# Performance work log

Hardware: AMD Instinct MI355X
Metric: run time of the kernel (lower is better)

## Reference

```python
import jax, jax.numpy as jnp
import numpy as np

B, T, C, H = 2, 2048, 1024, 16
N = C // H
MISS_ROWS = 128


def _rwkv7_scan(q, w_log, k, v, a, b):
    # all [B,T,H,N] float32 (bf16-rounded). RWKV7 delta-rule recurrence:
    #   S_t = S_{t-1} * diag(exp(w_t)) + (S_{t-1} a_t) b_t^T + v_t k_t^T
    #   o_t = S_t q_t   (state S has shape [B,H,Nv,Nk]; decay along k-dim)
    Bq, Tq, Hq, Nq = q.shape

    def step(S, inp):
        q_t, w_t, k_t, v_t, a_t, b_t = inp
        ew = jnp.exp(w_t)  # decay in (0,1) since w_log = -exp(...) < 0
        sa = jnp.einsum('bhvi,bhi->bhv', S, a_t)
        S = S * ew[:, :, None, :] + sa[..., None] * b_t[:, :, None, :] + v_t[..., None] * k_t[:, :, None, :]
        o = jnp.einsum('bhvj,bhj->bhv', S, q_t)
        return S, o

    xs = tuple(jnp.moveaxis(u, 1, 0) for u in (q, w_log, k, v, a, b))
    S0 = jnp.zeros((Bq, Hq, Nq, Nq), jnp.float32)
    _, o = jax.lax.scan(step, S0, xs)
    return jnp.moveaxis(o, 0, 1)  # [B,T,H,N]


def setup_inputs() -> dict:
    key = jax.random.key(0)
    ks = jax.random.split(key, 16)
    f32 = jnp.float32
    return {
        'residual': jax.random.normal(ks[0], (B, T, C), f32),
        'x': jax.random.normal(ks[1], (B, T, C), f32),
        'x0': jax.random.normal(ks[2], (B, T, C), f32),
        'dx0': jax.random.normal(ks[3], (B, T, C), f32),
        'Wq': jax.random.normal(ks[4], (C, C), f32) * 0.02,
        'Wk': jax.random.normal(ks[5], (C, C), f32) * 0.02,
        'Wv': jax.random.normal(ks[6], (C, C), f32) * 0.02,
        'Wproj': jax.random.normal(ks[7], (C, C), f32) * 0.02,
        'x_q': jax.random.uniform(ks[8], (1, 1, C), f32),
        'x_k': jax.random.uniform(ks[9], (1, 1, C), f32),
        'x_v': jax.random.uniform(ks[10], (1, 1, C), f32),
        'v0': 0.7 + 0.1 * jax.random.normal(ks[11], (1, 1, C), f32),
        'w0': -3.0 + 0.5 * jax.random.normal(ks[12], (1, 1, C), f32),
        'a0': 0.1 * jax.random.normal(ks[13], (1, 1, C), f32),
        'miss': jax.random.normal(ks[14], (MISS_ROWS, 4 * C), f32) * 0.02,
        'r_k': 0.1 * jax.random.normal(ks[15], (H, N), f32),
    }


def reference(residual, x, x0, dx0, Wq, Wk, Wv, Wproj, x_q, x_k, x_v, v0, w0, a0, miss, r_k):
    Bx, Tx, Cx = x.shape
    Hh, Nn = r_k.shape
    # token shift: dx_prev = x_{t-1} - x_t (zero-padded at t=0)
    dx_prev = jnp.concatenate([jnp.zeros_like(x[:, :1]), x[:, :-1]], axis=1) - x
    q = (x + dx_prev * x_q) @ Wq.T
    k = (x + dx_prev * x_k) @ Wk.T
    v = (x + dx_prev * x_v) @ Wv.T
    deltas = x[:, :, :miss.shape[0]] @ miss  # [B,T,4C]
    w_delta, v_delta, a_delta, g = jnp.split(deltas, 4, axis=-1)
    log_neglog_w = -jax.nn.softplus(-(w0 + w_delta)) - 0.5
    log_w = -jnp.exp(log_neglog_w)  # log decay, always < 0
    v_first = (x0 + dx0 * x_v) @ Wv.T
    v = v + (v_first - v) * jax.nn.sigmoid(v0 + v_delta)
    g = 1.0 + g
    a = jax.nn.sigmoid(a0 + a_delta)
    kh = k.reshape(Bx, Tx, Hh, Nn)
    kk = kh / jnp.maximum(jnp.linalg.norm(kh, axis=-1, keepdims=True), 1e-12)
    kk = kk.reshape(Bx, Tx, Cx)
    k = k * a
    z = -kk
    b = kk * a
    bf = lambda u: u.astype(jnp.bfloat16).astype(jnp.float32).reshape(Bx, Tx, Hh, Nn)
    qh, wh, kh2, vh, zh, bh = (bf(u) for u in (q, log_w, k, v, z, b))
    y = _rwkv7_scan(qh, wh, kh2, vh, zh, bh) * (float(Nn) ** -0.5)  # [B,T,H,N]
    xnorm = jnp.linalg.norm(x.reshape(Bx, Tx, Hh, Nn), axis=-1, keepdims=True)
    vnorm = jnp.linalg.norm(vh, axis=-1, keepdims=True)
    u = (1.0 - xnorm / (vnorm + 1e-12)) * jax.nn.sigmoid(r_k)
    y = (y + vh * u).reshape(Bx, Tx, Cx)
    y = y * g
    return residual + y @ Wproj.T
```

## Files before the change

### kernel.cpp

```cpp
#include <hip/hip_runtime.h>
#include <stdint.h>
#include <stddef.h>

#define B_ 2
#define T_ 2048
#define C_ 1024
#define H_ 16
#define N_ 64
#define M_ (B_*T_)
#define L_ 128
#define NC_ (T_/L_)

typedef unsigned short ushort_t;
typedef __attribute__((ext_vector_type(8))) __bf16 bf16x8;
typedef __attribute__((ext_vector_type(4))) float  f32x4;

__device__ __forceinline__ ushort_t f2bf(float x){
  uint32_t u = __float_as_uint(x);
  u += 0x7fffu + ((u >> 16) & 1u);
  return (ushort_t)(u >> 16);
}
__device__ __forceinline__ float bf2f(uint32_t hu){
  return __uint_as_float(hu << 16);
}
__device__ __forceinline__ void ldbf16x16(const ushort_t* p, float* o){
  uint4 u0 = *(const uint4*)p;
  uint4 u1 = *(const uint4*)(p+8);
  o[0]=bf2f(u0.x&0xffffu); o[1]=bf2f(u0.x>>16);
  o[2]=bf2f(u0.y&0xffffu); o[3]=bf2f(u0.y>>16);
  o[4]=bf2f(u0.z&0xffffu); o[5]=bf2f(u0.z>>16);
  o[6]=bf2f(u0.w&0xffffu); o[7]=bf2f(u0.w>>16);
  o[8]=bf2f(u1.x&0xffffu); o[9]=bf2f(u1.x>>16);
  o[10]=bf2f(u1.y&0xffffu); o[11]=bf2f(u1.y>>16);
  o[12]=bf2f(u1.z&0xffffu); o[13]=bf2f(u1.z>>16);
  o[14]=bf2f(u1.w&0xffffu); o[15]=bf2f(u1.w>>16);
}
__device__ __forceinline__ float quad_sum(float v){
  float a = __int_as_float(__builtin_amdgcn_mov_dpp(__float_as_int(v), 0xB1, 0xF, 0xF, true));
  v += a;
  float b = __int_as_float(__builtin_amdgcn_mov_dpp(__float_as_int(v), 0x4E, 0xF, 0xF, true));
  return v + b;
}

__device__ __forceinline__ ushort4 mixq4(float4 a, float4 p, float4 c){
  ushort4 o;
  o.x = f2bf(fmaf(p.x - a.x, c.x, a.x));
  o.y = f2bf(fmaf(p.y - a.y, c.y, a.y));
  o.z = f2bf(fmaf(p.z - a.z, c.z, a.z));
  o.w = f2bf(fmaf(p.w - a.w, c.w, a.w));
  return o;
}
__global__ __launch_bounds__(256) void prep_all(
    const float* __restrict__ x, const float* __restrict__ x0,
    const float* __restrict__ dx0,
    const float* __restrict__ xq, const float* __restrict__ xk,
    const float* __restrict__ xv,
    const float* __restrict__ Wq, const float* __restrict__ Wk,
    const float* __restrict__ Wv, const float* __restrict__ Wp,
    const float* __restrict__ miss,
    ushort_t* __restrict__ Aq, ushort_t* __restrict__ Ak,
    ushort_t* __restrict__ Av, ushort_t* __restrict__ Axf,
    ushort_t* __restrict__ Xb,
    ushort_t* __restrict__ Wb, ushort_t* __restrict__ Wpb,
    ushort_t* __restrict__ missT)
{
  __shared__ ushort_t tile[128][66];
  const int blk = blockIdx.x;
  const int tid = threadIdx.x;
  if (blk < 4096){
    const int idx = blk*256 + tid;
    const int col4 = idx & 255;
    const int i = idx >> 8;
    const int t = i & (T_-1);
    float4 a = ((const float4*)x)[idx];
    float4 p = {0.f,0.f,0.f,0.f};
    if (t > 0) p = ((const float4*)x)[idx - 256];
    float4 cq = ((const float4*)xq)[col4];
    float4 ck = ((const float4*)xk)[col4];
    float4 cv = ((const float4*)xv)[col4];
    ((ushort4*)Aq)[idx] = mixq4(a, p, cq);
    ((ushort4*)Ak)[idx] = mixq4(a, p, ck);
    ((ushort4*)Av)[idx] = mixq4(a, p, cv);
    float4 z = ((const float4*)x0)[idx];
    float4 d = ((const float4*)dx0)[idx];
    ushort4 of;
    of.x = f2bf(fmaf(d.x, cv.x, z.x));
    of.y = f2bf(fmaf(d.y, cv.y, z.y));
    of.z = f2bf(fmaf(d.z, cv.z, z.z));
    of.w = f2bf(fmaf(d.w, cv.w, z.w));
    ((ushort4*)Axf)[idx] = of;
    ushort4 ob = {f2bf(a.x), f2bf(a.y), f2bf(a.z), f2bf(a.w)};
    ((ushort4*)Xb)[idx] = ob;
  } else if (blk < 4096 + 5*1024){
    const int y = (blk - 4096) >> 10;
    const float* src = (y==0)?Wq:(y==1)?Wk:(y<4)?Wv:Wp;
    ushort_t* dst = (y<4) ? Wb + (size_t)y*C_*C_ : Wpb;
    const int idx = ((blk - 4096) & 1023)*256 + tid;
    float4 v = ((const float4*)src)[idx];
    ushort4 o = {f2bf(v.x), f2bf(v.y), f2bf(v.z), f2bf(v.w)};
    ((ushort4*)dst)[idx] = o;
  } else {
    const int j0 = (blk - 4096 - 5*1024)*64;
#pragma unroll
    for (int rep=0; rep<8; rep++){
      int k = rep*16 + (tid>>4);
      int jj = (tid&15)*4;
      float4 v = *(const float4*)&miss[(size_t)k*4096 + j0 + jj];
      tile[k][jj+0]=f2bf(v.x); tile[k][jj+1]=f2bf(v.y);
      tile[k][jj+2]=f2bf(v.z); tile[k][jj+3]=f2bf(v.w);
    }
    __syncthreads();
#pragma unroll
    for (int rep=0; rep<8; rep++){
      int j = tid>>2;
      int kk = (tid&3)*32 + rep*4;
      ushort4 o = {tile[kk+0][j], tile[kk+1][j], tile[kk+2][j], tile[kk+3][j]};
      *(ushort4*)&missT[(size_t)(j0+j)*128 + kk] = o;
    }
  }
}

__global__ __launch_bounds__(256, 2) void mfma_gemm(
    const ushort_t* __restrict__ Ab, int lda, int64_t Asz,
    const ushort_t* __restrict__ Bbp, int ldb, int64_t Bsz,
    void* __restrict__ Cb, int ldc, int64_t Csz, int c_bf16,
    const float* __restrict__ resid, int K)
{
  const ushort_t* A  = Ab  + (size_t)blockIdx.z * Asz;
  const ushort_t* Bm = Bbp + (size_t)blockIdx.z * Bsz;
  const int i0 = blockIdx.y * 128;
  const int j0 = blockIdx.x * 128;
  const int tid = threadIdx.x;
  const int lane = tid & 63;
  const int w = tid >> 6;
  const int wm = w & 1, wn = w >> 1;

  __shared__ ushort_t As[128*32];
  __shared__ ushort_t Bs[128*32];

  f32x4 acc[4][4];
#pragma unroll
  for (int i=0;i<4;i++)
#pragma unroll
    for (int j=0;j<4;j++) acc[i][j] = (f32x4){0.f,0.f,0.f,0.f};

  const int lr = lane >> 2;
  const int ls = lane & 3;
  const ushort_t* ga = A  + (size_t)(i0 + w*32 + lr)*lda + ls*8;
  const ushort_t* gb = Bm + (size_t)(j0 + w*32 + lr)*ldb + ls*8;
  const int lm = lane & 15, lq = lane >> 4;

  for (int k0 = 0; k0 < K; k0 += 32){
    __syncthreads();
#pragma unroll
    for (int p=0;p<2;p++){
      __builtin_amdgcn_global_load_lds(
        (const __attribute__((address_space(1))) void*)(ga + (size_t)p*16*lda + k0),
        (__attribute__((address_space(3))) void*)&As[(w*32 + p*16)*32], 16, 0, 0);
      __builtin_amdgcn_global_load_lds(
        (const __attribute__((address_space(1))) void*)(gb + (size_t)p*16*ldb + k0),
        (__attribute__((address_space(3))) void*)&Bs[(w*32 + p*16)*32], 16, 0, 0);
    }
    __syncthreads();
    bf16x8 af[4], bfr[4];
#pragma unroll
    for (int i=0;i<4;i++)
      af[i] = *(const bf16x8*)&As[(wm*64 + i*16 + lm)*32 + lq*8];
#pragma unroll
    for (int j=0;j<4;j++)
      bfr[j] = *(const bf16x8*)&Bs[(wn*64 + j*16 + lm)*32 + lq*8];
#pragma unroll
    for (int i=0;i<4;i++)
#pragma unroll
      for (int j=0;j<4;j++)
        acc[i][j] = __builtin_amdgcn_mfma_f32_16x16x32_bf16(af[i], bfr[j], acc[i][j], 0, 0, 0);
  }

  if (!c_bf16){
    float* C = (float*)Cb + (size_t)blockIdx.z * Csz;
#pragma unroll
    for (int i=0;i<4;i++)
#pragma unroll
      for (int j=0;j<4;j++)
#pragma unroll
        for (int r=0;r<4;r++){
          const int row = i0 + wm*64 + i*16 + lq*4 + r;
          const int col = j0 + wn*64 + j*16 + lm;
          float v = acc[i][j][r];
          if (resid) v += resid[(size_t)row*ldc + col];
          C[(size_t)row*ldc + col] = v;
        }
  } else {
    ushort_t* C = (ushort_t*)Cb + (size_t)blockIdx.z * Csz;
#pragma unroll
    for (int i=0;i<4;i++)
#pragma unroll
      for (int j=0;j<4;j++)
#pragma unroll
        for (int r=0;r<4;r++){
          const int row = i0 + wm*64 + i*16 + lq*4 + r;
          const int col = j0 + wn*64 + j*16 + lm;
          C[(size_t)row*ldc + col] = f2bf(acc[i][j][r]);
        }
  }
}

__global__ __launch_bounds__(256) void fuse_kernel(
    const float* __restrict__ qm, const float* __restrict__ km,
    const float* __restrict__ vm, const float* __restrict__ vfm,
    const ushort_t* __restrict__ del, const float* __restrict__ x,
    const float* __restrict__ w0, const float* __restrict__ v0,
    const float* __restrict__ a0,
    uint32_t* __restrict__ packed, float* __restrict__ gout,
    float* __restrict__ ratio)
{
  const int lane = threadIdx.x & 63;
  const int ht = blockIdx.x*4 + (threadIdx.x >> 6);
  const int i = ht >> 4;
  const int h = ht & 15;
  const int c = h*64 + lane;
  const size_t ic = (size_t)i*C_ + c;
  float qv = qm[ic], kv = km[ic], vv = vm[ic], vfv = vfm[ic], xv = x[ic];
  const size_t d0 = (size_t)i*4*C_ + c;
  float wd = bf2f(del[d0]), vd = bf2f(del[d0+C_]);
  float ad = bf2f(del[d0+2*C_]), gd = bf2f(del[d0+3*C_]);

  float z1 = -(w0[c]+wd);
  float sp = fmaxf(z1, 0.f) + log1pf(expf(-fabsf(z1)));
  float logw = -expf(-sp - 0.5f);
  float sv = 1.f/(1.f+expf(-(v0[c]+vd)));
  vv = vv + (vfv - vv)*sv;
  float gv = 1.f + gd;
  float av = 1.f/(1.f+expf(-(a0[c]+ad)));

  ushort_t vr_u = f2bf(vv);
  float vrf = bf2f(vr_u);

  float ksq = kv*kv, xsq = xv*xv, vsq = vrf*vrf;
#pragma unroll
  for (int off=32; off>0; off>>=1){
    ksq += __shfl_xor(ksq, off, 64);
    xsq += __shfl_xor(xsq, off, 64);
    vsq += __shfl_xor(vsq, off, 64);
  }
  float kn = sqrtf(ksq);
  float kkn = kv / fmaxf(kn, 1e-12f);
  float k2 = kv*av;
  float zv = -kkn;
  float bv = kkn*av;

  uint32_t p0 = (uint32_t)f2bf(logw) | ((uint32_t)f2bf(zv) << 16);
  uint32_t p1 = (uint32_t)f2bf(bv)   | ((uint32_t)f2bf(k2) << 16);
  uint32_t p2 = (uint32_t)f2bf(qv)   | ((uint32_t)vr_u << 16);
  uint32_t* pb = packed + ((size_t)ht*64 + lane)*3;
  pb[0]=p0; pb[1]=p1; pb[2]=p2;
  gout[ic] = gv;
  if (lane == 0)
    ratio[ht] = 1.f - sqrtf(xsq)/(sqrtf(vsq)+1e-12f);
}


__global__ __launch_bounds__(512, 4) void chunk_mdp_kernel(
    const uint32_t* __restrict__ packed,
    float* __restrict__ phi, float* __restrict__ cc, float* __restrict__ md)
{
  const int tid  = threadIdx.x;
  const int role = tid >> 8;
  const int row  = (tid >> 2) & 63;
  const int qr   = tid & 3;

  __shared__ float ewS[8][N_], zS[8][N_], bS[8][N_], kS[8][N_], qS[8][N_], vS[8][N_];

  const int g  = blockIdx.x;
  const int cx = g & (NC_-1), bh = g >> 4;
  const int b = bh >> 4, h = bh & 15;
  const size_t pbase = ((size_t)(b*T_ + cx*L_)*H_ + h)*64;

  const int ls = tid >> 6;
  const int ld = tid & 63;

  uint32_t pu0, pu1, pu2;
  {
    size_t ap = (pbase + (size_t)ls*(H_*64) + ld)*3;
    pu0 = packed[ap]; pu1 = packed[ap+1]; pu2 = packed[ap+2];
  }

  float R[16];
  if (role == 0){
#pragma unroll
    for (int i=0;i<16;i++) R[i] = (qr*16+i == row) ? 1.f : 0.f;
  } else {
#pragma unroll
    for (int i=0;i<16;i++) R[i] = 0.f;
  }

  for (int tg = 0; tg < L_; tg += 8){
    __syncthreads();
    ewS[ls][ld] = __expf(bf2f(pu0 & 0xffffu));
    zS[ls][ld]  = bf2f(pu0 >> 16);
    bS[ls][ld]  = bf2f(pu1 & 0xffffu);
    kS[ls][ld]  = bf2f(pu1 >> 16);
    qS[ls][ld]  = bf2f(pu2 & 0xffffu);
    vS[ls][ld]  = bf2f(pu2 >> 16);
    if (tg + 8 < L_){
      size_t ap = (pbase + (size_t)(tg+8+ls)*(H_*64) + ld)*3;
      pu0 = packed[ap]; pu1 = packed[ap+1]; pu2 = packed[ap+2];
    }
    __syncthreads();
#pragma unroll 1
    for (int ss=0; ss<8; ss++){
      const float* zr = &zS[ss][qr*16];
      float s_ = 0.f;
#pragma unroll
      for (int i4=0;i4<4;i4++){
        float4 z4 = *(const float4*)&zr[i4*4];
        s_ = fmaf(R[i4*4+0], z4.x, s_);
        s_ = fmaf(R[i4*4+1], z4.y, s_);
        s_ = fmaf(R[i4*4+2], z4.z, s_);
        s_ = fmaf(R[i4*4+3], z4.w, s_);
      }
      s_ = quad_sum(s_);
      const float* er = &ewS[ss][qr*16];
      const float* br = &bS[ss][qr*16];
      const float* qrp = &qS[ss][qr*16];
      float o = 0.f;
      if (role == 0){
#pragma unroll
        for (int i4=0;i4<4;i4++){
          float4 e4 = *(const float4*)&er[i4*4];
          float4 b4 = *(const float4*)&br[i4*4];
          float4 q4 = *(const float4*)&qrp[i4*4];
          float t;
          t = fmaf(R[i4*4+0], e4.x, s_*b4.x); R[i4*4+0]=t; o = fmaf(t, q4.x, o);
          t = fmaf(R[i4*4+1], e4.y, s_*b4.y); R[i4*4+1]=t; o = fmaf(t, q4.y, o);
          t = fmaf(R[i4*4+2], e4.z, s_*b4.z); R[i4*4+2]=t; o = fmaf(t, q4.z, o);
          t = fmaf(R[i4*4+3], e4.w, s_*b4.w); R[i4*4+3]=t; o = fmaf(t, q4.w, o);
        }
      } else {
        const float* kr = &kS[ss][qr*16];
        const float vr = vS[ss][row];
#pragma unroll
        for (int i4=0;i4<4;i4++){
          float4 e4 = *(const float4*)&er[i4*4];
          float4 b4 = *(const float4*)&br[i4*4];
          float4 q4 = *(const float4*)&qrp[i4*4];
          float4 k4 = *(const float4*)&kr[i4*4];
          float t;
          t = fmaf(R[i4*4+0], e4.x, fmaf(s_, b4.x, vr*k4.x)); R[i4*4+0]=t; o = fmaf(t, q4.x, o);
          t = fmaf(R[i4*4+1], e4.y, fmaf(s_, b4.y, vr*k4.y)); R[i4*4+1]=t; o = fmaf(t, q4.y, o);
          t = fmaf(R[i4*4+2], e4.z, fmaf(s_, b4.z, vr*k4.z)); R[i4*4+2]=t; o = fmaf(t, q4.z, o);
          t = fmaf(R[i4*4+3], e4.w, fmaf(s_, b4.w, vr*k4.w)); R[i4*4+3]=t; o = fmaf(t, q4.w, o);
        }
      }
      o = quad_sum(o);
      if (qr == 0)
        md[((size_t)g*L_ + tg+ss)*128 + role*64 + row] = o;
    }
  }
  float* dst = (role == 0) ? phi : cc;
  const size_t base = (size_t)g*4096 + (size_t)row*64 + qr*16;
#pragma unroll
  for (int i4=0;i4<4;i4++)
    *(float4*)&dst[base + i4*4] = (float4){R[i4*4+0],R[i4*4+1],R[i4*4+2],R[i4*4+3]};
}

__global__ __launch_bounds__(256) void chunk_state_kernel(
    const float* __restrict__ phi, const float* __restrict__ cc,
    float* __restrict__ sstart)
{
  const int bh = blockIdx.x;
  const int tid = threadIdx.x;
  const int rb = tid >> 4;
  const int cq = tid & 15;
  __shared__ float Sld[64][65];
  __shared__ float Fld[64][68];
  float acc[4][4];
#pragma unroll
  for (int m=0;m<4;m++)
#pragma unroll
    for (int i=0;i<4;i++) acc[m][i] = 0.f;
#pragma unroll
  for (int m=0;m<4;m++){
    float4 z4 = {0.f,0.f,0.f,0.f};
    *(float4*)&Sld[rb+16*m][cq*4] = z4;
  }
  const float* pc = phi + (size_t)bh*NC_*4096;
  const float* cb = cc  + (size_t)bh*NC_*4096;
  float4 pf[4], pcc[4];
#pragma unroll
  for (int p=0;p<4;p++) pf[p] = *(const float4*)&pc[(size_t)p*1024 + tid*4];
#pragma unroll
  for (int m=0;m<4;m++) pcc[m] = *(const float4*)&cb[(size_t)(rb+16*m)*64 + cq*4];

  for (int c=0;c<NC_;c++){
    __syncthreads();
#pragma unroll
    for (int p=0;p<4;p++){
      int f = p*1024 + tid*4;
      *(float4*)&Fld[f>>6][f&63] = pf[p];
    }
    float na[4][4];
#pragma unroll
    for (int m=0;m<4;m++){
      na[m][0]=pcc[m].x; na[m][1]=pcc[m].y; na[m][2]=pcc[m].z; na[m][3]=pcc[m].w;
    }
#pragma unroll
    for (int m=0;m<4;m++){
      float4 so = {acc[m][0],acc[m][1],acc[m][2],acc[m][3]};
      *(float4*)&sstart[(size_t)(bh*NC_+c)*4096 + (size_t)(rb+16*m)*64 + cq*4] = so;
    }
    if (c+1 < NC_){
#pragma unroll
      for (int p=0;p<4;p++) pf[p] = *(const float4*)&pc[(size_t)(c+1)*4096 + p*1024 + tid*4];
#pragma unroll
      for (int m=0;m<4;m++) pcc[m] = *(const float4*)&cb[(size_t)(c+1)*4096 + (size_t)(rb+16*m)*64 + cq*4];
    }
    __syncthreads();
#pragma unroll 1
    for (int k0=0;k0<64;k0+=4){
      float4 sr[4];
#pragma unroll
      for (int m=0;m<4;m++) sr[m] = *(const float4*)&Sld[rb+16*m][k0];
      const float4 f0 = *(const float4*)&Fld[k0+0][cq*4];
      const float4 f1 = *(const float4*)&Fld[k0+1][cq*4];
      const float4 f2 = *(const float4*)&Fld[k0+2][cq*4];
      const float4 f3 = *(const float4*)&Fld[k0+3][cq*4];
#pragma unroll
      for (int m=0;m<4;m++){
        na[m][0] = fmaf(sr[m].x, f0.x, na[m][0]); na[m][0] = fmaf(sr[m].y, f1.x, na[m][0]);
        na[m][0] = fmaf(sr[m].z, f2.x, na[m][0]); na[m][0] = fmaf(sr[m].w, f3.x, na[m][0]);
        na[m][1] = fmaf(sr[m].x, f0.y, na[m][1]); na[m][1] = fmaf(sr[m].y, f1.y, na[m][1]);
        na[m][1] = fmaf(sr[m].z, f2.y, na[m][1]); na[m][1] = fmaf(sr[m].w, f3.y, na[m][1]);
        na[m][2] = fmaf(sr[m].x, f0.z, na[m][2]); na[m][2] = fmaf(sr[m].y, f1.z, na[m][2]);
        na[m][2] = fmaf(sr[m].z, f2.z, na[m][2]); na[m][2] = fmaf(sr[m].w, f3.z, na[m][2]);
        na[m][3] = fmaf(sr[m].x, f0.w, na[m][3]); na[m][3] = fmaf(sr[m].y, f1.w, na[m][3]);
        na[m][3] = fmaf(sr[m].z, f2.w, na[m][3]); na[m][3] = fmaf(sr[m].w, f3.w, na[m][3]);
      }
    }
    __syncthreads();
#pragma unroll
    for (int m=0;m<4;m++){
      float4 so = {na[m][0],na[m][1],na[m][2],na[m][3]};
      *(float4*)&Sld[rb+16*m][cq*4] = so;
#pragma unroll
      for (int i=0;i<4;i++) acc[m][i] = na[m][i];
    }
  }
}

__global__ __launch_bounds__(256) void chunk_emit_kernel(
    const uint32_t* __restrict__ packed, const float* __restrict__ ratio,
    const float* __restrict__ g, const float* __restrict__ rk,
    const float* __restrict__ sstart, const float* __restrict__ md,
    ushort_t* __restrict__ y)
{
  const int blk = blockIdx.x;
  const int c  = blk & (NC_-1);
  const int bh = blk >> 4;
  const int b = bh >> 4, h = bh & 15;
  const int tid = threadIdx.x;
  const int v = tid & 63;
  const int tg = tid >> 6;

  float4 sr[16];
  const float4* sp = (const float4*)(sstart + (size_t)blk*4096 + (size_t)v*64);
#pragma unroll
  for (int f=0;f<16;f++) sr[f] = sp[f];
  const float sigrk = 1.f/(1.f+__expf(-rk[h*64+v]));

#pragma unroll 1
  for (int ss=0; ss<32; ss++){
    const int t = tg*32 + ss;
    const int token = b*T_ + c*L_ + t;
    const float* mrow = md + ((size_t)blk*L_ + t)*128;
    float o0=0.f,o1=0.f,o2=0.f,o3=0.f;
#pragma unroll
    for (int f=0;f<16;f+=4){
      float4 m0 = ((const float4*)mrow)[f+0];
      float4 m1 = ((const float4*)mrow)[f+1];
      float4 m2 = ((const float4*)mrow)[f+2];
      float4 m3 = ((const float4*)mrow)[f+3];
      o0 = fmaf(sr[f+0].x,m0.x, fmaf(sr[f+0].y,m0.y, fmaf(sr[f+0].z,m0.z, fmaf(sr[f+0].w,m0.w, o0))));
      o1 = fmaf(sr[f+1].x,m1.x, fmaf(sr[f+1].y,m1.y, fmaf(sr[f+1].z,m1.z, fmaf(sr[f+1].w,m1.w, o1))));
      o2 = fmaf(sr[f+2].x,m2.x, fmaf(sr[f+2].y,m2.y, fmaf(sr[f+2].z,m2.z, fmaf(sr[f+2].w,m2.w, o2))));
      o3 = fmaf(sr[f+3].x,m3.x, fmaf(sr[f+3].y,m3.y, fmaf(sr[f+3].z,m3.z, fmaf(sr[f+3].w,m3.w, o3))));
    }
    float o = ((o0+o1)+(o2+o3)) + mrow[64 + v];
    const float vt = bf2f(packed[(((size_t)token*H_ + h)*64 + v)*3 + 2] >> 16);
    const float uv = ratio[(size_t)token*H_ + h];
    const float gv = g[(size_t)token*C_ + h*64 + v];
    y[(size_t)token*C_ + h*64 + v] = f2bf((o*0.125f + vt*uv*sigrk)*gv);
  }
}

extern "C" void kernel_launch(void* const* d_in, const int* in_sizes, int n_in,
                              void* d_out, int out_size, void* d_ws, size_t ws_size,
                              hipStream_t stream)
{
  const float* residual = (const float*)d_in[0];
  const float* x    = (const float*)d_in[1];
  const float* x0   = (const float*)d_in[2];
  const float* dx0  = (const float*)d_in[3];
  const float* Wq   = (const float*)d_in[4];
  const float* Wk   = (const float*)d_in[5];
  const float* Wv   = (const float*)d_in[6];
  const float* Wpr  = (const float*)d_in[7];
  const float* x_q  = (const float*)d_in[8];
  const float* x_k  = (const float*)d_in[9];
  const float* x_v  = (const float*)d_in[10];
  const float* v0   = (const float*)d_in[11];
  const float* w0   = (const float*)d_in[12];
  const float* a0   = (const float*)d_in[13];
  const float* miss = (const float*)d_in[14];
  const float* rk   = (const float*)d_in[15];
  float* out = (float*)d_out;

  char* ws = (char*)d_ws;
  const size_t MB = (size_t)1 << 20;
  float*    q_m    = (float*)(ws + 0*MB);
  float*    k_m    = (float*)(ws + 16*MB);
  float*    v_m    = (float*)(ws + 32*MB);
  float*    vf_m   = (float*)(ws + 48*MB);
  ushort_t* delb   = (ushort_t*)(ws + 64*MB);
  ushort_t* Ab     = (ushort_t*)(ws + 96*MB);
  ushort_t* Xb     = (ushort_t*)(ws + 128*MB);
  ushort_t* Wb     = (ushort_t*)(ws + 136*MB);
  uint32_t* packed = (uint32_t*)(ws + 96*MB);
  float*    g_m    = (float*)(ws + 144*MB);
  ushort_t* Wpb    = (ushort_t*)(ws + 160*MB);
  ushort_t* missT  = (ushort_t*)(ws + 162*MB);
  float*    ratio  = (float*)(ws + 163*MB);
  float*    phi    = (float*)(ws + 0*MB);
  float*    cc     = (float*)(ws + 16*MB);
  float*    sstart = (float*)(ws + 32*MB);
  ushort_t* yb     = (ushort_t*)(ws + 48*MB);
  float*    mdbuf  = (float*)(ws + 64*MB);

  ushort_t* Aq  = Ab + 0*(size_t)M_*C_;
  ushort_t* Ak  = Ab + 1*(size_t)M_*C_;
  ushort_t* Av  = Ab + 2*(size_t)M_*C_;
  ushort_t* Axf = Ab + 3*(size_t)M_*C_;

  dim3 blk(256);
  prep_all<<<4096 + 5*1024 + 64, blk, 0, stream>>>(
      x, x0, dx0, x_q, x_k, x_v, Wq, Wk, Wv, Wpr, miss,
      Aq, Ak, Av, Axf, Xb, Wb, Wpb, missT);
  mfma_gemm<<<dim3(C_/128, M_/128, 4), blk, 0, stream>>>(
      Ab, C_, (int64_t)M_*C_, Wb, C_, (int64_t)C_*C_,
      q_m, C_, (int64_t)M_*C_, 0, nullptr, C_);
  mfma_gemm<<<dim3(4*C_/128, M_/128, 1), blk, 0, stream>>>(
      Xb, C_, 0, missT, 128, 0, delb, 4*C_, 0, 1, nullptr, 128);
  fuse_kernel<<<M_*H_/4, blk, 0, stream>>>(q_m, k_m, v_m, vf_m, delb, x, w0, v0, a0, packed, g_m, ratio);
  chunk_mdp_kernel<<<B_*H_*NC_, dim3(512), 0, stream>>>(packed, phi, cc, mdbuf);
  chunk_state_kernel<<<B_*H_, blk, 0, stream>>>(phi, cc, sstart);
  chunk_emit_kernel<<<B_*H_*NC_, blk, 0, stream>>>(packed, ratio, g_m, rk, sstart, mdbuf, yb);
  mfma_gemm<<<dim3(C_/128, M_/128, 1), blk, 0, stream>>>(
      yb, C_, 0, Wpb, C_, 0, out, C_, 0, 0, residual, C_);
}
```

Measured before the change: 507.6 us.

## Double-buffer chunk inputs in LDS and shorten dot-product dependency chains

The chunk recurrence kernel now keeps two LDS buffers for the per-step inputs. The next group of 8 timesteps is written while the current group is computed, which removes one of the two barriers per group. The serial fma accumulation chains for the s and o dot products are split into four partial sums reduced as a tree, and the inner step loop is fully unrolled to expose more instruction-level parallelism. Costs are doubled LDS usage, which may limit occupancy at 4 blocks per CU, plus a small rounding-order change in the sums.

```diff
diff --git a/kernel.cpp b/kernel.cpp
--- a/kernel.cpp
+++ b/kernel.cpp
@@ -22,18 +22,6 @@
 }
 __device__ __forceinline__ float bf2f(uint32_t hu){
   return __uint_as_float(hu << 16);
-}
-__device__ __forceinline__ void ldbf16x16(const ushort_t* p, float* o){
-  uint4 u0 = *(const uint4*)p;
-  uint4 u1 = *(const uint4*)(p+8);
-  o[0]=bf2f(u0.x&0xffffu); o[1]=bf2f(u0.x>>16);
-  o[2]=bf2f(u0.y&0xffffu); o[3]=bf2f(u0.y>>16);
-  o[4]=bf2f(u0.z&0xffffu); o[5]=bf2f(u0.z>>16);
-  o[6]=bf2f(u0.w&0xffffu); o[7]=bf2f(u0.w>>16);
-  o[8]=bf2f(u1.x&0xffffu); o[9]=bf2f(u1.x>>16);
-  o[10]=bf2f(u1.y&0xffffu); o[11]=bf2f(u1.y>>16);
-  o[12]=bf2f(u1.z&0xffffu); o[13]=bf2f(u1.z>>16);
-  o[14]=bf2f(u1.w&0xffffu); o[15]=bf2f(u1.w>>16);
 }
 __device__ __forceinline__ float quad_sum(float v){
   float a = __int_as_float(__builtin_amdgcn_mov_dpp(__float_as_int(v), 0xB1, 0xF, 0xF, true));
@@ -269,7 +257,7 @@
   const int row  = (tid >> 2) & 63;
   const int qr   = tid & 3;
 
-  __shared__ float ewS[8][N_], zS[8][N_], bS[8][N_], kS[8][N_], qS[8][N_], vS[8][N_];
+  __shared__ float ewS[2][8][N_], zS[2][8][N_], bS[2][8][N_], kS[2][8][N_], qS[2][8][N_], vS[2][8][N_];
 
   const int g  = blockIdx.x;
   const int cx = g & (NC_-1), bh = g >> 4;
@@ -284,6 +272,16 @@
     size_t ap = (pbase + (size_t)ls*(H_*64) + ld)*3;
     pu0 = packed[ap]; pu1 = packed[ap+1]; pu2 = packed[ap+2];
   }
+  ewS[0][ls][ld] = __expf(bf2f(pu0 & 0xffffu));
+  zS[0][ls][ld]  = bf2f(pu0 >> 16);
+  bS[0][ls][ld]  = bf2f(pu1 & 0xffffu);
+  kS[0][ls][ld]  = bf2f(pu1 >> 16);
+  qS[0][ls][ld]  = bf2f(pu2 & 0xffffu);
+  vS[0][ls][ld]  = bf2f(pu2 >> 16);
+  {
+    size_t ap = (pbase + (size_t)(8+ls)*(H_*64) + ld)*3;
+    pu0 = packed[ap]; pu1 = packed[ap+1]; pu2 = packed[ap+2];
+  }
 
   float R[16];
   if (role == 0){
@@ -294,68 +292,75 @@
     for (int i=0;i<16;i++) R[i] = 0.f;
   }
 
-  for (int tg = 0; tg < L_; tg += 8){
-    __syncthreads();
-    ewS[ls][ld] = __expf(bf2f(pu0 & 0xffffu));
-    zS[ls][ld]  = bf2f(pu0 >> 16);
-    bS[ls][ld]  = bf2f(pu1 & 0xffffu);
-    kS[ls][ld]  = bf2f(pu1 >> 16);
-    qS[ls][ld]  = bf2f(pu2 & 0xffffu);
-    vS[ls][ld]  = bf2f(pu2 >> 16);
-    if (tg + 8 < L_){
-      size_t ap = (pbase + (size_t)(tg+8+ls)*(H_*64) + ld)*3;
-      pu0 = packed[ap]; pu1 = packed[ap+1]; pu2 = packed[ap+2];
-    }
-    __syncthreads();
+  const size_t mdb = (size_t)g*L_*128 + (size_t)(role*64 + row);
+  __syncthreads();
+
+  const int NG = L_/8;
 #pragma unroll 1
+  for (int grp = 0; grp < NG; ++grp){
+    const int cur = grp & 1, nxt = cur ^ 1;
+    if (grp + 1 < NG){
+      ewS[nxt][ls][ld] = __expf(bf2f(pu0 & 0xffffu));
+      zS[nxt][ls][ld]  = bf2f(pu0 >> 16);
+      bS[nxt][ls][ld]  = bf2f(pu1 & 0xffffu);
+      kS[nxt][ls][ld]  = bf2f(pu1 >> 16);
+      qS[nxt][ls][ld]  = bf2f(pu2 & 0xffffu);
+      vS[nxt][ls][ld]  = bf2f(pu2 >> 16);
+      if (grp + 2 < NG){
+        size_t ap = (pbase + (size_t)((grp+2)*8+ls)*(H_*64) + ld)*3;
+        pu0 = packed[ap]; pu1 = packed[ap+1]; pu2 = packed[ap+2];
+      }
+    }
+#pragma unroll
     for (int ss=0; ss<8; ss++){
-      const float* zr = &zS[ss][qr*16];
-      float s_ = 0.f;
+      const float* zr = &zS[cur][ss][qr*16];
+      float sa[4];
 #pragma unroll
       for (int i4=0;i4<4;i4++){
         float4 z4 = *(const float4*)&zr[i4*4];
-        s_ = fmaf(R[i4*4+0], z4.x, s_);
-        s_ = fmaf(R[i4*4+1], z4.y, s_);
-        s_ = fmaf(R[i4*4+2], z4.z, s_);
-        s_ = fmaf(R[i4*4+3], z4.w, s_);
+        sa[i4] = fmaf(R[i4*4+3], z4.w, fmaf(R[i4*4+2], z4.z,
+                 fmaf(R[i4*4+1], z4.y, R[i4*4+0]*z4.x)));
       }
-      s_ = quad_sum(s_);
-      const float* er = &ewS[ss][qr*16];
-      const float* br = &bS[ss][qr*16];
-      const float* qrp = &qS[ss][qr*16];
-      float o = 0.f;
+      const float s_ = quad_sum((sa[0]+sa[1])+(sa[2]+sa[3]));
+      const float* er = &ewS[cur][ss][qr*16];
+      const float* br = &bS[cur][ss][qr*16];
+      const float* qp = &qS[cur][ss][qr*16];
+      float oa[4];
       if (role == 0){
 #pragma unroll
         for (int i4=0;i4<4;i4++){
           float4 e4 = *(const float4*)&er[i4*4];
           float4 b4 = *(const float4*)&br[i4*4];
-          float4 q4 = *(const float4*)&qrp[i4*4];
-          float t;
-          t = fmaf(R[i4*4+0], e4.x, s_*b4.x); R[i4*4+0]=t; o = fmaf(t, q4.x, o);
-          t = fmaf(R[i4*4+1], e4.y, s_*b4.y); R[i4*4+1]=t; o = fmaf(t, q4.y, o);
-          t = fmaf(R[i4*4+2], e4.z, s_*b4.z); R[i4*4+2]=t; o = fmaf(t, q4.z, o);
-          t = fmaf(R[i4*4+3], e4.w, s_*b4.w); R[i4*4+3]=t; o = fmaf(t, q4.w, o);
+          float4 q4 = *(const float4*)&qp[i4*4];
+          float t0 = fmaf(R[i4*4+0], e4.x, s_*b4.x);
+          float t1 = fmaf(R[i4*4+1], e4.y, s_*b4.y);
+          float t2 = fmaf(R[i4*4+2], e4.z, s_*b4.z);
+          float t3 = fmaf(R[i4*4+3], e4.w, s_*b4.w);
+          R[i4*4+0]=t0; R[i4*4+1]=t1; R[i4*4+2]=t2; R[i4*4+3]=t3;
+          oa[i4] = fmaf(t3, q4.w, fmaf(t2, q4.z, fmaf(t1, q4.y, t0*q4.x)));
         }
       } else {
-        const float* kr = &kS[ss][qr*16];
-        const float vr = vS[ss][row];
+        const float* kr = &kS[cur][ss][qr*16];
+        const float vr = vS[cur][ss][row];
 #pragma unroll
         for (int i4=0;i4<4;i4++){
           float4 e4 = *(const float4*)&er[i4*4];
           float4 b4 = *(const float4*)&br[i4*4];
-          float4 q4 = *(const float4*)&qrp[i4*4];
+          float4 q4 = *(const float4*)&qp[i4*4];
           float4 k4 = *(const float4*)&kr[i4*4];
-          float t;
-          t = fmaf(R[i4*4+0], e4.x, fmaf(s_, b4.x, vr*k4.x)); R[i4*4+0]=t; o = fmaf(t, q4.x, o);
-          t = fmaf(R[i4*4+1], e4.y, fmaf(s_, b4.y, vr*k4.y)); R[i4*4+1]=t; o = fmaf(t, q4.y, o);
-          t = fmaf(R[i4*4+2], e4.z, fmaf(s_, b4.z, vr*k4.z)); R[i4*4+2]=t; o = fmaf(t, q4.z, o);
-          t = fmaf(R[i4*4+3], e4.w, fmaf(s_, b4.w, vr*k4.w)); R[i4*4+3]=t; o = fmaf(t, q4.w, o);
+          float t0 = fmaf(R[i4*4+0], e4.x, fmaf(s_, b4.x, vr*k4.x));
+          float t1 = fmaf(R[i4*4+1], e4.y, fmaf(s_, b4.y, vr*k4.y));
+          float t2 = fmaf(R[i4*4+2], e4.z, fmaf(s_, b4.z, vr*k4.z));
+          float t3 = fmaf(R[i4*4+3], e4.w, fmaf(s_, b4.w, vr*k4.w));
+          R[i4*4+0]=t0; R[i4*4+1]=t1; R[i4*4+2]=t2; R[i4*4+3]=t3;
+          oa[i4] = fmaf(t3, q4.w, fmaf(t2, q4.z, fmaf(t1, q4.y, t0*q4.x)));
         }
       }
-      o = quad_sum(o);
+      float o = quad_sum((oa[0]+oa[1])+(oa[2]+oa[3]));
       if (qr == 0)
-        md[((size_t)g*L_ + tg+ss)*128 + role*64 + row] = o;
-    }
+        md[mdb + (size_t)(grp*8+ss)*128] = o;
+    }
+    __syncthreads();
   }
   float* dst = (role == 0) ? phi : cc;
   const size_t base = (size_t)g*4096 + (size_t)row*64 + qr*16;
```

Measured after the change: 524.9 us. 1.03x slower.

## Split chunk recurrence rows across 8 lanes with 1024-thread blocks

Applied to the files above, without the earlier changes.

The chunk_mdp kernel now uses 1024 threads per block, with each state row handled by 8 lanes holding 8 columns each instead of 4 lanes holding 16. Reductions use a three-step DPP sum across 8 lanes, and the inner time loop is fully unrolled with split accumulators to shorten the serial dependency chain. This shortens the per-thread sequential work in the recurrence. In exchange it adds a reduction step, the loads are predicated to the first 512 threads, and occupancy pressure rises with the larger blocks.

```diff
diff --git a/kernel.cpp b/kernel.cpp
--- a/kernel.cpp
+++ b/kernel.cpp
@@ -23,23 +23,19 @@
 __device__ __forceinline__ float bf2f(uint32_t hu){
   return __uint_as_float(hu << 16);
 }
-__device__ __forceinline__ void ldbf16x16(const ushort_t* p, float* o){
-  uint4 u0 = *(const uint4*)p;
-  uint4 u1 = *(const uint4*)(p+8);
-  o[0]=bf2f(u0.x&0xffffu); o[1]=bf2f(u0.x>>16);
-  o[2]=bf2f(u0.y&0xffffu); o[3]=bf2f(u0.y>>16);
-  o[4]=bf2f(u0.z&0xffffu); o[5]=bf2f(u0.z>>16);
-  o[6]=bf2f(u0.w&0xffffu); o[7]=bf2f(u0.w>>16);
-  o[8]=bf2f(u1.x&0xffffu); o[9]=bf2f(u1.x>>16);
-  o[10]=bf2f(u1.y&0xffffu); o[11]=bf2f(u1.y>>16);
-  o[12]=bf2f(u1.z&0xffffu); o[13]=bf2f(u1.z>>16);
-  o[14]=bf2f(u1.w&0xffffu); o[15]=bf2f(u1.w>>16);
-}
 __device__ __forceinline__ float quad_sum(float v){
   float a = __int_as_float(__builtin_amdgcn_mov_dpp(__float_as_int(v), 0xB1, 0xF, 0xF, true));
   v += a;
   float b = __int_as_float(__builtin_amdgcn_mov_dpp(__float_as_int(v), 0x4E, 0xF, 0xF, true));
   return v + b;
+}
+__device__ __forceinline__ float sum8(float v){
+  float a = __int_as_float(__builtin_amdgcn_mov_dpp(__float_as_int(v), 0xB1, 0xF, 0xF, true));
+  v += a;
+  float b = __int_as_float(__builtin_amdgcn_mov_dpp(__float_as_int(v), 0x4E, 0xF, 0xF, true));
+  v += b;
+  float c = __int_as_float(__builtin_amdgcn_mov_dpp(__float_as_int(v), 0x141, 0xF, 0xF, true));
+  return v + c;
 }
 
 __device__ __forceinline__ ushort4 mixq4(float4 a, float4 p, float4 c){
@@ -260,14 +256,14 @@
 }
 
 
-__global__ __launch_bounds__(512, 4) void chunk_mdp_kernel(
+__global__ __launch_bounds__(1024, 8) void chunk_mdp_kernel(
     const uint32_t* __restrict__ packed,
     float* __restrict__ phi, float* __restrict__ cc, float* __restrict__ md)
 {
   const int tid  = threadIdx.x;
-  const int role = tid >> 8;
-  const int row  = (tid >> 2) & 63;
-  const int qr   = tid & 3;
+  const int role = tid >> 9;
+  const int row  = (tid >> 3) & 63;
+  const int cg   = tid & 7;
 
   __shared__ float ewS[8][N_], zS[8][N_], bS[8][N_], kS[8][N_], qS[8][N_], vS[8][N_];
 
@@ -279,89 +275,93 @@
   const int ls = tid >> 6;
   const int ld = tid & 63;
 
-  uint32_t pu0, pu1, pu2;
-  {
+  uint32_t pu0=0, pu1=0, pu2=0;
+  if (tid < 512){
     size_t ap = (pbase + (size_t)ls*(H_*64) + ld)*3;
     pu0 = packed[ap]; pu1 = packed[ap+1]; pu2 = packed[ap+2];
   }
 
-  float R[16];
+  float R[8];
   if (role == 0){
 #pragma unroll
-    for (int i=0;i<16;i++) R[i] = (qr*16+i == row) ? 1.f : 0.f;
+    for (int i=0;i<8;i++) R[i] = (cg*8+i == row) ? 1.f : 0.f;
   } else {
 #pragma unroll
-    for (int i=0;i<16;i++) R[i] = 0.f;
-  }
-
-  for (int tg = 0; tg < L_; tg += 8){
-    __syncthreads();
-    ewS[ls][ld] = __expf(bf2f(pu0 & 0xffffu));
-    zS[ls][ld]  = bf2f(pu0 >> 16);
-    bS[ls][ld]  = bf2f(pu1 & 0xffffu);
-    kS[ls][ld]  = bf2f(pu1 >> 16);
-    qS[ls][ld]  = bf2f(pu2 & 0xffffu);
-    vS[ls][ld]  = bf2f(pu2 >> 16);
-    if (tg + 8 < L_){
-      size_t ap = (pbase + (size_t)(tg+8+ls)*(H_*64) + ld)*3;
-      pu0 = packed[ap]; pu1 = packed[ap+1]; pu2 = packed[ap+2];
-    }
-    __syncthreads();
+    for (int i=0;i<8;i++) R[i] = 0.f;
+  }
+
+  float* mdp = md + (size_t)g*L_*128 + (role*64 + row);
+
+  const int NG = L_/8;
 #pragma unroll 1
+  for (int grp = 0; grp < NG; ++grp){
+    __syncthreads();
+    if (tid < 512){
+      ewS[ls][ld] = __expf(bf2f(pu0 & 0xffffu));
+      zS[ls][ld]  = bf2f(pu0 >> 16);
+      bS[ls][ld]  = bf2f(pu1 & 0xffffu);
+      kS[ls][ld]  = bf2f(pu1 >> 16);
+      qS[ls][ld]  = bf2f(pu2 & 0xffffu);
+      vS[ls][ld]  = bf2f(pu2 >> 16);
+      if (grp + 1 < NG){
+        size_t ap = (pbase + (size_t)((grp+1)*8+ls)*(H_*64) + ld)*3;
+        pu0 = packed[ap]; pu1 = packed[ap+1]; pu2 = packed[ap+2];
+      }
+    }
+    __syncthreads();
+#pragma unroll
     for (int ss=0; ss<8; ss++){
-      const float* zr = &zS[ss][qr*16];
-      float s_ = 0.f;
-#pragma unroll
-      for (int i4=0;i4<4;i4++){
-        float4 z4 = *(const float4*)&zr[i4*4];
-        s_ = fmaf(R[i4*4+0], z4.x, s_);
-        s_ = fmaf(R[i4*4+1], z4.y, s_);
-        s_ = fmaf(R[i4*4+2], z4.z, s_);
-        s_ = fmaf(R[i4*4+3], z4.w, s_);
+      const float4 z0 = *(const float4*)&zS[ss][cg*8];
+      const float4 z1 = *(const float4*)&zS[ss][cg*8+4];
+      float sza = fmaf(R[3], z0.w, fmaf(R[2], z0.z, fmaf(R[1], z0.y, R[0]*z0.x)));
+      float szb = fmaf(R[7], z1.w, fmaf(R[6], z1.z, fmaf(R[5], z1.y, R[4]*z1.x)));
+      const float s_ = sum8(sza + szb);
+      const float4 e0 = *(const float4*)&ewS[ss][cg*8];
+      const float4 e1 = *(const float4*)&ewS[ss][cg*8+4];
+      const float4 b0 = *(const float4*)&bS[ss][cg*8];
+      const float4 b1 = *(const float4*)&bS[ss][cg*8+4];
+      const float4 q0 = *(const float4*)&qS[ss][cg*8];
+      const float4 q1 = *(const float4*)&qS[ss][cg*8+4];
+      float oa, ob;
+      if (role == 0){
+        float t0 = fmaf(R[0], e0.x, s_*b0.x);
+        float t1 = fmaf(R[1], e0.y, s_*b0.y);
+        float t2 = fmaf(R[2], e0.z, s_*b0.z);
+        float t3 = fmaf(R[3], e0.w, s_*b0.w);
+        float t4 = fmaf(R[4], e1.x, s_*b1.x);
+        float t5 = fmaf(R[5], e1.y, s_*b1.y);
+        float t6 = fmaf(R[6], e1.z, s_*b1.z);
+        float t7 = fmaf(R[7], e1.w, s_*b1.w);
+        R[0]=t0; R[1]=t1; R[2]=t2; R[3]=t3;
+        R[4]=t4; R[5]=t5; R[6]=t6; R[7]=t7;
+        oa = fmaf(t3, q0.w, fmaf(t2, q0.z, fmaf(t1, q0.y, t0*q0.x)));
+        ob = fmaf(t7, q1.w, fmaf(t6, q1.z, fmaf(t5, q1.y, t4*q1.x)));
+      } else {
+        const float4 k0 = *(const float4*)&kS[ss][cg*8];
+        const float4 k1 = *(const float4*)&kS[ss][cg*8+4];
+        const float vr = vS[ss][row];
+        float t0 = fmaf(R[0], e0.x, fmaf(s_, b0.x, vr*k0.x));
+        float t1 = fmaf(R[1], e0.y, fmaf(s_, b0.y, vr*k0.y));
+        float t2 = fmaf(R[2], e0.z, fmaf(s_, b0.z, vr*k0.z));
+        float t3 = fmaf(R[3], e0.w, fmaf(s_, b0.w, vr*k0.w));
+        float t4 = fmaf(R[4], e1.x, fmaf(s_, b1.x, vr*k1.x));
+        float t5 = fmaf(R[5], e1.y, fmaf(s_, b1.y, vr*k1.y));
+        float t6 = fmaf(R[6], e1.z, fmaf(s_, b1.z, vr*k1.z));
+        float t7 = fmaf(R[7], e1.w, fmaf(s_, b1.w, vr*k1.w));
+        R[0]=t0; R[1]=t1; R[2]=t2; R[3]=t3;
+        R[4]=t4; R[5]=t5; R[6]=t6; R[7]=t7;
+        oa = fmaf(t3, q0.w, fmaf(t2, q0.z, fmaf(t1, q0.y, t0*q0.x)));
+        ob = fmaf(t7, q1.w, fmaf(t6, q1.z, fmaf(t5, q1.y, t4*q1.x)));
       }
-      s_ = quad_sum(s_);
-      const float* er = &ewS[ss][qr*16];
-      const float* br = &bS[ss][qr*16];
-      const float* qrp = &qS[ss][qr*16];
-      float o = 0.f;
-      if (role == 0){
-#pragma unroll
-        for (int i4=0;i4<4;i4++){
-          float4 e4 = *(const float4*)&er[i4*4];
-          float4 b4 = *(const float4*)&br[i4*4];
-          float4 q4 = *(const float4*)&qrp[i4*4];
-          float t;
-          t = fmaf(R[i4*4+0], e4.x, s_*b4.x); R[i4*4+0]=t; o = fmaf(t, q4.x, o);
-          t = fmaf(R[i4*4+1], e4.y, s_*b4.y); R[i4*4+1]=t; o = fmaf(t, q4.y, o);
-          t = fmaf(R[i4*4+2], e4.z, s_*b4.z); R[i4*4+2]=t; o = fmaf(t, q4.z, o);
-          t = fmaf(R[i4*4+3], e4.w, s_*b4.w); R[i4*4+3]=t; o = fmaf(t, q4.w, o);
-        }
-      } else {
-        const float* kr = &kS[ss][qr*16];
-        const float vr = vS[ss][row];
-#pragma unroll
-        for (int i4=0;i4<4;i4++){
-          float4 e4 = *(const float4*)&er[i4*4];
-          float4 b4 = *(const float4*)&br[i4*4];
-          float4 q4 = *(const float4*)&qrp[i4*4];
-          float4 k4 = *(const float4*)&kr[i4*4];
-          float t;
-          t = fmaf(R[i4*4+0], e4.x, fmaf(s_, b4.x, vr*k4.x)); R[i4*4+0]=t; o = fmaf(t, q4.x, o);
-          t = fmaf(R[i4*4+1], e4.y, fmaf(s_, b4.y, vr*k4.y)); R[i4*4+1]=t; o = fmaf(t, q4.y, o);
-          t = fmaf(R[i4*4+2], e4.z, fmaf(s_, b4.z, vr*k4.z)); R[i4*4+2]=t; o = fmaf(t, q4.z, o);
-          t = fmaf(R[i4*4+3], e4.w, fmaf(s_, b4.w, vr*k4.w)); R[i4*4+3]=t; o = fmaf(t, q4.w, o);
-        }
-      }
-      o = quad_sum(o);
-      if (qr == 0)
-        md[((size_t)g*L_ + tg+ss)*128 + role*64 + row] = o;
+      float o = sum8(oa + ob);
+      if (cg == 0)
+        mdp[(size_t)(grp*8+ss)*128] = o;
     }
   }
   float* dst = (role == 0) ? phi : cc;
-  const size_t base = (size_t)g*4096 + (size_t)row*64 + qr*16;
-#pragma unroll
-  for (int i4=0;i4<4;i4++)
-    *(float4*)&dst[base + i4*4] = (float4){R[i4*4+0],R[i4*4+1],R[i4*4+2],R[i4*4+3]};
+  const size_t base = (size_t)g*4096 + (size_t)row*64 + cg*8;
+  *(float4*)&dst[base]     = (float4){R[0],R[1],R[2],R[3]};
+  *(float4*)&dst[base + 4] = (float4){R[4],R[5],R[6],R[7]};
 }
 
 __global__ __launch_bounds__(256) void chunk_state_kernel(
@@ -551,7 +551,7 @@
   mfma_gemm<<<dim3(4*C_/128, M_/128, 1), blk, 0, stream>>>(
       Xb, C_, 0, missT, 128, 0, delb, 4*C_, 0, 1, nullptr, 128);
   fuse_kernel<<<M_*H_/4, blk, 0, stream>>>(q_m, k_m, v_m, vf_m, delb, x, w0, v0, a0, packed, g_m, ratio);
-  chunk_mdp_kernel<<<B_*H_*NC_, dim3(512), 0, stream>>>(packed, phi, cc, mdbuf);
+  chunk_mdp_kernel<<<B_*H_*NC_, dim3(1024), 0, stream>>>(packed, phi, cc, mdbuf);
   chunk_state_kernel<<<B_*H_, blk, 0, stream>>>(phi, cc, sstart);
   chunk_emit_kernel<<<B_*H_*NC_, blk, 0, stream>>>(packed, ratio, g_m, rk, sstart, mdbuf, yb);
   mfma_gemm<<<dim3(C_/128, M_/128, 1), blk, 0, stream>>>(
```

Measured after the change: 539.0 us. 1.06x slower.

## Split chunk state recurrence across row blocks to raise parallelism

Applied to the files above, without the earlier changes.

The sequential inter-chunk state propagation kernel previously ran one block per (batch, head) and had each thread compute 4x4 outputs over all 64 state rows. It now launches 4 blocks per (batch, head), each owning 16 rows, which is valid because each state row evolves independently through the shared transition matrix. This raises the launch from 32 to 128 blocks and shortens the per-thread serial work on the critical path. In exchange, each block reloads the full 64x64 transition matrix per chunk, so global reads of phi increase fourfold. An unused helper is also removed.

```diff
diff --git a/kernel.cpp b/kernel.cpp
--- a/kernel.cpp
+++ b/kernel.cpp
@@ -22,18 +22,6 @@
 }
 __device__ __forceinline__ float bf2f(uint32_t hu){
   return __uint_as_float(hu << 16);
-}
-__device__ __forceinline__ void ldbf16x16(const ushort_t* p, float* o){
-  uint4 u0 = *(const uint4*)p;
-  uint4 u1 = *(const uint4*)(p+8);
-  o[0]=bf2f(u0.x&0xffffu); o[1]=bf2f(u0.x>>16);
-  o[2]=bf2f(u0.y&0xffffu); o[3]=bf2f(u0.y>>16);
-  o[4]=bf2f(u0.z&0xffffu); o[5]=bf2f(u0.z>>16);
-  o[6]=bf2f(u0.w&0xffffu); o[7]=bf2f(u0.w>>16);
-  o[8]=bf2f(u1.x&0xffffu); o[9]=bf2f(u1.x>>16);
-  o[10]=bf2f(u1.y&0xffffu); o[11]=bf2f(u1.y>>16);
-  o[12]=bf2f(u1.z&0xffffu); o[13]=bf2f(u1.z>>16);
-  o[14]=bf2f(u1.w&0xffffu); o[15]=bf2f(u1.w>>16);
 }
 __device__ __forceinline__ float quad_sum(float v){
   float a = __int_as_float(__builtin_amdgcn_mov_dpp(__float_as_int(v), 0xB1, 0xF, 0xF, true));
@@ -368,29 +356,22 @@
     const float* __restrict__ phi, const float* __restrict__ cc,
     float* __restrict__ sstart)
 {
-  const int bh = blockIdx.x;
+  const int mq = blockIdx.x;
+  const int bh = blockIdx.y;
   const int tid = threadIdx.x;
   const int rb = tid >> 4;
   const int cq = tid & 15;
-  __shared__ float Sld[64][65];
+  const int row = mq*16 + rb;
+  __shared__ float Sld[16][65];
   __shared__ float Fld[64][68];
-  float acc[4][4];
-#pragma unroll
-  for (int m=0;m<4;m++)
-#pragma unroll
-    for (int i=0;i<4;i++) acc[m][i] = 0.f;
-#pragma unroll
-  for (int m=0;m<4;m++){
-    float4 z4 = {0.f,0.f,0.f,0.f};
-    *(float4*)&Sld[rb+16*m][cq*4] = z4;
-  }
+  float acc[4] = {0.f, 0.f, 0.f, 0.f};
+  *(float4*)&Sld[rb][cq*4] = (float4){0.f,0.f,0.f,0.f};
   const float* pc = phi + (size_t)bh*NC_*4096;
   const float* cb = cc  + (size_t)bh*NC_*4096;
-  float4 pf[4], pcc[4];
+  float4 pf[4], pcc;
 #pragma unroll
   for (int p=0;p<4;p++) pf[p] = *(const float4*)&pc[(size_t)p*1024 + tid*4];
-#pragma unroll
-  for (int m=0;m<4;m++) pcc[m] = *(const float4*)&cb[(size_t)(rb+16*m)*64 + cq*4];
+  pcc = *(const float4*)&cb[(size_t)row*64 + cq*4];
 
   for (int c=0;c<NC_;c++){
     __syncthreads();
@@ -399,52 +380,35 @@
       int f = p*1024 + tid*4;
       *(float4*)&Fld[f>>6][f&63] = pf[p];
     }
-    float na[4][4];
-#pragma unroll
-    for (int m=0;m<4;m++){
-      na[m][0]=pcc[m].x; na[m][1]=pcc[m].y; na[m][2]=pcc[m].z; na[m][3]=pcc[m].w;
-    }
-#pragma unroll
-    for (int m=0;m<4;m++){
-      float4 so = {acc[m][0],acc[m][1],acc[m][2],acc[m][3]};
-      *(float4*)&sstart[(size_t)(bh*NC_+c)*4096 + (size_t)(rb+16*m)*64 + cq*4] = so;
-    }
+    float na[4] = {pcc.x, pcc.y, pcc.z, pcc.w};
+    *(float4*)&sstart[(size_t)(bh*NC_+c)*4096 + (size_t)row*64 + cq*4] =
+        (float4){acc[0],acc[1],acc[2],acc[3]};
     if (c+1 < NC_){
 #pragma unroll
       for (int p=0;p<4;p++) pf[p] = *(const float4*)&pc[(size_t)(c+1)*4096 + p*1024 + tid*4];
-#pragma unroll
-      for (int m=0;m<4;m++) pcc[m] = *(const float4*)&cb[(size_t)(c+1)*4096 + (size_t)(rb+16*m)*64 + cq*4];
+      pcc = *(const float4*)&cb[(size_t)(c+1)*4096 + (size_t)row*64 + cq*4];
     }
     __syncthreads();
 #pragma unroll 1
     for (int k0=0;k0<64;k0+=4){
-      float4 sr[4];
-#pragma unroll
-      for (int m=0;m<4;m++) sr[m] = *(const float4*)&Sld[rb+16*m][k0];
+      const float4 sr = *(const float4*)&Sld[rb][k0];
       const float4 f0 = *(const float4*)&Fld[k0+0][cq*4];
       const float4 f1 = *(const float4*)&Fld[k0+1][cq*4];
       const float4 f2 = *(const float4*)&Fld[k0+2][cq*4];
       const float4 f3 = *(const float4*)&Fld[k0+3][cq*4];
-#pragma unroll
-      for (int m=0;m<4;m++){
-        na[m][0] = fmaf(sr[m].x, f0.x, na[m][0]); na[m][0] = fmaf(sr[m].y, f1.x, na[m][0]);
-        na[m][0] = fmaf(sr[m].z, f2.x, na[m][0]); na[m][0] = fmaf(sr[m].w, f3.x, na[m][0]);
-        na[m][1] = fmaf(sr[m].x, f0.y, na[m][1]); na[m][1] = fmaf(sr[m].y, f1.y, na[m][1]);
-        na[m][1] = fmaf(sr[m].z, f2.y, na[m][1]); na[m][1] = fmaf(sr[m].w, f3.y, na[m][1]);
-        na[m][2] = fmaf(sr[m].x, f0.z, na[m][2]); na[m][2] = fmaf(sr[m].y, f1.z, na[m][2]);
-        na[m][2] = fmaf(sr[m].z, f2.z, na[m][2]); na[m][2] = fmaf(sr[m].w, f3.z, na[m][2]);
-        na[m][3] = fmaf(sr[m].x, f0.w, na[m][3]); na[m][3] = fmaf(sr[m].y, f1.w, na[m][3]);
-        na[m][3] = fmaf(sr[m].z, f2.w, na[m][3]); na[m][3] = fmaf(sr[m].w, f3.w, na[m][3]);
-      }
-    }
-    __syncthreads();
-#pragma unroll
-    for (int m=0;m<4;m++){
-      float4 so = {na[m][0],na[m][1],na[m][2],na[m][3]};
-      *(float4*)&Sld[rb+16*m][cq*4] = so;
-#pragma unroll
-      for (int i=0;i<4;i++) acc[m][i] = na[m][i];
-    }
+      na[0] = fmaf(sr.x, f0.x, na[0]); na[0] = fmaf(sr.y, f1.x, na[0]);
+      na[0] = fmaf(sr.z, f2.x, na[0]); na[0] = fmaf(sr.w, f3.x, na[0]);
+      na[1] = fmaf(sr.x, f0.y, na[1]); na[1] = fmaf(sr.y, f1.y, na[1]);
+      na[1] = fmaf(sr.z, f2.y, na[1]); na[1] = fmaf(sr.w, f3.y, na[1]);
+      na[2] = fmaf(sr.x, f0.z, na[2]); na[2] = fmaf(sr.y, f1.z, na[2]);
+      na[2] = fmaf(sr.z, f2.z, na[2]); na[2] = fmaf(sr.w, f3.z, na[2]);
+      na[3] = fmaf(sr.x, f0.w, na[3]); na[3] = fmaf(sr.y, f1.w, na[3]);
+      na[3] = fmaf(sr.z, f2.w, na[3]); na[3] = fmaf(sr.w, f3.w, na[3]);
+    }
+    __syncthreads();
+    *(float4*)&Sld[rb][cq*4] = (float4){na[0],na[1],na[2],na[3]};
+#pragma unroll
+    for (int i=0;i<4;i++) acc[i] = na[i];
   }
 }
 
@@ -552,7 +516,7 @@
       Xb, C_, 0, missT, 128, 0, delb, 4*C_, 0, 1, nullptr, 128);
   fuse_kernel<<<M_*H_/4, blk, 0, stream>>>(q_m, k_m, v_m, vf_m, delb, x, w0, v0, a0, packed, g_m, ratio);
   chunk_mdp_kernel<<<B_*H_*NC_, dim3(512), 0, stream>>>(packed, phi, cc, mdbuf);
-  chunk_state_kernel<<<B_*H_, blk, 0, stream>>>(phi, cc, sstart);
+  chunk_state_kernel<<<dim3(4, B_*H_), blk, 0, stream>>>(phi, cc, sstart);
   chunk_emit_kernel<<<B_*H_*NC_, blk, 0, stream>>>(packed, ratio, g_m, rk, sstart, mdbuf, yb);
   mfma_gemm<<<dim3(C_/128, M_/128, 1), blk, 0, stream>>>(
       yb, C_, 0, Wpb, C_, 0, out, C_, 0, 0, residual, C_);
```

New measurement: 485.5 us. 1.05x faster.
